# Optimization experiments

Hardware: AMD Instinct MI355X
Metric: run time of the kernel (lower is better)

The kernel has to match this reference:

```python
import jax, jax.numpy as jnp
import numpy as np
import math

D_MODEL = 1024
N_HEADS = 16
D_K = D_MODEL // N_HEADS
HIDDEN = 4096
R_SOFTPLUS_0 = 1.442695041
EPS = 1e-6


def setup_inputs() -> dict:
    key = jax.random.key(0)
    ks = jax.random.split(key, 16)
    B, S = 4, 2048
    s = 0.02
    inp = {
        "inputs": jax.random.normal(ks[0], (B, S, D_MODEL), jnp.float32),
        "mask": jnp.zeros((1, 1, S, S), jnp.float32),
        # RmsNorm (direct_scale=True -> init 1.0)
        "rms_scale": jnp.ones((D_MODEL,), jnp.float32),
        # attention projections (torch Linear: y = x @ W.T + b)
        "Wq": jax.random.normal(ks[1], (D_MODEL, D_MODEL), jnp.float32) * s,
        "bq": jnp.zeros((D_MODEL,), jnp.float32),
        "Wk": jax.random.normal(ks[2], (D_MODEL, D_MODEL), jnp.float32) * s,
        "bk": jnp.zeros((D_MODEL,), jnp.float32),
        "Wv": jax.random.normal(ks[3], (D_MODEL, D_MODEL), jnp.float32) * s,
        "bv": jnp.zeros((D_MODEL,), jnp.float32),
        "per_dim_scale": jnp.zeros((D_K,), jnp.float32),
        "Wpost": jax.random.normal(ks[4], (D_MODEL, D_MODEL), jnp.float32) * s,
        "bpost": jnp.zeros((D_MODEL,), jnp.float32),
        # FFN LayerNorm (direct_scale=False -> scale param init 0, effective 1+scale)
        "ln_scale": jnp.zeros((D_MODEL,), jnp.float32),
        "ln_bias": jnp.zeros((D_MODEL,), jnp.float32),
        "W1": jax.random.normal(ks[5], (HIDDEN, D_MODEL), jnp.float32) * s,
        "b1": jnp.zeros((HIDDEN,), jnp.float32),
        "W2": jax.random.normal(ks[6], (D_MODEL, HIDDEN), jnp.float32) * s,
        "b2": jnp.zeros((D_MODEL,), jnp.float32),
    }
    return inp


def _rms_norm(x, scale):
    ms = jnp.mean(x * x, axis=-1, keepdims=True)
    return x * jax.lax.rsqrt(ms + EPS) * scale


def _layer_norm(x, scale, bias):
    mean = jnp.mean(x, axis=-1, keepdims=True)
    var = jnp.mean((x - mean) ** 2, axis=-1, keepdims=True)
    return (x - mean) * jax.lax.rsqrt(var + EPS) * (1.0 + scale) + bias


def reference(inputs, mask, rms_scale, Wq, bq, Wk, bk, Wv, bv, per_dim_scale,
              Wpost, bpost, ln_scale, ln_bias, W1, b1, W2, b2):
    B, S, _ = inputs.shape
    x = _rms_norm(inputs, rms_scale)
    # projections -> [B, H, S, Dk]
    def split_heads(t):
        return t.reshape(B, S, N_HEADS, D_K).transpose(0, 2, 1, 3)
    q = split_heads(x @ Wq.T + bq)
    k = split_heads(x @ Wk.T + bk)
    v = split_heads(x @ Wv.T + bv)
    # PerDimScale: (r_softplus_0 / sqrt(d_k)) * softplus(param)
    scale = (R_SOFTPLUS_0 / math.sqrt(D_K)) * jax.nn.softplus(per_dim_scale)
    q = q * scale
    attn = jnp.einsum("bhqd,bhkd->bhqk", q, k) + mask
    attn = jax.nn.softmax(attn, axis=-1)
    out = jnp.einsum("bhqk,bhkd->bhqd", attn, v)
    out = out.transpose(0, 2, 1, 3).reshape(B, S, D_MODEL)
    attn_out = out @ Wpost.T + bpost
    h = attn_out + inputs  # residual (dropout=0)
    # FeedForward with pre-LayerNorm and residual
    y = _layer_norm(h, ln_scale, ln_bias)
    y = jax.nn.relu(y @ W1.T + b1)
    y = y @ W2.T + b2
    return y + h
```

## Files before the change

kernel.cpp:

```cpp
#include <hip/hip_runtime.h>
#include <hip/hip_bf16.h>

typedef unsigned short u16;
typedef __attribute__((ext_vector_type(8))) short short8;
typedef __attribute__((ext_vector_type(4))) float floatx4;

#define R_PDS 0.18033688f
#define LOG2E 1.4426950408889634f

__device__ __forceinline__ float bf2f(u16 u) {
    union { float f; unsigned int i; } c; c.i = ((unsigned int)u) << 16; return c.f;
}
__device__ __forceinline__ u16 f2b(float f) {
    union { float f; unsigned int i; } c; c.f = f;
    unsigned int r = c.i + 0x7fffu + ((c.i >> 16) & 1u);
    return (u16)(r >> 16);
}
__device__ __forceinline__ unsigned int pk2(float a, float b) {
    __hip_bfloat162 h = __float22bfloat162_rn(float2{a, b});
    unsigned int u; __builtin_memcpy(&u, &h, 4); return u;
}

__device__ __forceinline__ void async16(const u16* g, u16* l) {
    __builtin_amdgcn_global_load_lds(
        (const __attribute__((address_space(1))) unsigned int*)g,
        (__attribute__((address_space(3))) unsigned int*)l, 16, 0, 0);
}

__global__ __launch_bounds__(256) void f2b_all_k(const float* __restrict__ Wq, const float* __restrict__ Wk,
                                                 const float* __restrict__ Wv, const float* __restrict__ Wp,
                                                 const float* __restrict__ W1, const float* __restrict__ W2,
                                                 u16* __restrict__ Wqkvb, u16* __restrict__ Wpb,
                                                 u16* __restrict__ W1b,  u16* __restrict__ W2b,
                                                 int* flag) {
    int bid = blockIdx.x;
    if (bid == 0 && threadIdx.x == 0) *flag = 0;
    const float* src; u16* dst; int off;
    if      (bid < 1024) { src = Wq; dst = Wqkvb;                off = bid; }
    else if (bid < 2048) { src = Wk; dst = Wqkvb + 1024 * 1024;  off = bid - 1024; }
    else if (bid < 3072) { src = Wv; dst = Wqkvb + 2048 * 1024;  off = bid - 2048; }
    else if (bid < 4096) { src = Wp; dst = Wpb;                  off = bid - 3072; }
    else if (bid < 8192) { src = W1; dst = W1b;                  off = bid - 4096; }
    else                 { src = W2; dst = W2b;                  off = bid - 8192; }
    int i = off * 256 + threadIdx.x;
    float4 v = ((const float4*)src)[i];
    uint2 w; w.x = pk2(v.x, v.y); w.y = pk2(v.z, v.w);
    ((uint2*)dst)[i] = w;
}

__global__ __launch_bounds__(256) void mask_any_k(const float* __restrict__ mask, int* flag) {
    int i = blockIdx.x * 256 + threadIdx.x;
    uint4 u = ((const uint4*)mask)[i];
    unsigned int v = (u.x | u.y | u.z | u.w) & 0x7fffffffu;
    if (v) atomicOr(flag, 1);
}

__global__ __launch_bounds__(256) void rmsnorm_k(const float* __restrict__ in,
                                                 const float* __restrict__ gscale,
                                                 u16* __restrict__ out) {
    int row = blockIdx.x;
    int t = threadIdx.x, lane = t & 63, wave = t >> 6;
    const float* x = in + (size_t)row * 1024;
    float4 v = *(const float4*)(x + t * 4);
    float ss = v.x*v.x + v.y*v.y + v.z*v.z + v.w*v.w;
    for (int o = 1; o < 64; o <<= 1) ss += __shfl_xor(ss, o, 64);
    __shared__ float red[4];
    if (lane == 0) red[wave] = ss;
    __syncthreads();
    float tot = red[0] + red[1] + red[2] + red[3];
    float inv = rsqrtf(tot * (1.0f / 1024.0f) + 1e-6f);
    float4 s = *(const float4*)(gscale + t * 4);
    uint2 w;
    w.x = pk2(v.x * inv * s.x, v.y * inv * s.y);
    w.y = pk2(v.z * inv * s.z, v.w * inv * s.w);
    *(uint2*)(out + (size_t)row * 1024 + t * 4) = w;
}

__global__ __launch_bounds__(256) void layernorm_k(const u16* __restrict__ in,
                                                   const float* __restrict__ gs,
                                                   const float* __restrict__ gb,
                                                   u16* __restrict__ out) {
    int row = blockIdx.x;
    int t = threadIdx.x, lane = t & 63, wave = t >> 6;
    const u16* x = in + (size_t)row * 1024;
    uint2 u = *(const uint2*)(x + t * 4);
    float v0 = bf2f((u16)(u.x & 0xffff)), v1 = bf2f((u16)(u.x >> 16));
    float v2 = bf2f((u16)(u.y & 0xffff)), v3 = bf2f((u16)(u.y >> 16));
    float s1 = v0 + v1 + v2 + v3;
    float s2 = v0*v0 + v1*v1 + v2*v2 + v3*v3;
    for (int o = 1; o < 64; o <<= 1) { s1 += __shfl_xor(s1, o, 64); s2 += __shfl_xor(s2, o, 64); }
    __shared__ float r1[4], r2[4];
    if (lane == 0) { r1[wave] = s1; r2[wave] = s2; }
    __syncthreads();
    float mean = (r1[0] + r1[1] + r1[2] + r1[3]) * (1.0f / 1024.0f);
    float var  = (r2[0] + r2[1] + r2[2] + r2[3]) * (1.0f / 1024.0f) - mean * mean;
    var = fmaxf(var, 0.0f);
    float inv = rsqrtf(var + 1e-6f);
    float4 sc = *(const float4*)(gs + t * 4);
    float4 bb = *(const float4*)(gb + t * 4);
    uint2 w;
    w.x = pk2((v0 - mean) * inv * (1.0f + sc.x) + bb.x,
              (v1 - mean) * inv * (1.0f + sc.y) + bb.y);
    w.y = pk2((v2 - mean) * inv * (1.0f + sc.z) + bb.z,
              (v3 - mean) * inv * (1.0f + sc.w) + bb.w);
    *(uint2*)(out + (size_t)row * 1024 + t * 4) = w;
}

__device__ __forceinline__ void gemm8_core(const u16* __restrict__ A, const u16* __restrict__ B,
                                           int K, int NG, int m0, int n0,
                                           u16* lds, floatx4 (&acc)[8][4]) {
    const int t = threadIdx.x, wave = t >> 6, lane = t & 63;
    const int quad = lane >> 4, ln = lane & 15;
    const int wave_m = wave >> 2, wave_n = wave & 3;

    const int rowS = t >> 3;
    const int srcb = ((t & 7) * 16) ^ (((t >> 3) & 7) << 4);
    const u16* Ab = A + (size_t)(m0 + rowS) * K + (srcb >> 1);
    const u16* Bb = B + (size_t)(n0 + rowS) * K + (srcb >> 1);
    const size_t rstep = (size_t)64 * K;
    const size_t hstep = (size_t)128 * K;
    const int ldw = wave * 512;

    #define STAGE_A8(buf, h, kt) do { \
        u16* _l = lds + (buf) * 32768 + (h) * 8192 + ldw; \
        const u16* _g = Ab + (size_t)(h) * hstep + (kt); \
        async16(_g, _l); async16(_g + rstep, _l + 4096); } while (0)
    #define STAGE_B8(buf, h, kt) do { \
        u16* _l = lds + (buf) * 32768 + 16384 + (h) * 8192 + ldw; \
        const u16* _g = Bb + (size_t)(h) * hstep + (kt); \
        async16(_g, _l); async16(_g + rstep, _l + 4096); } while (0)

    #define RD8(base, lr, ks) \
        (*(const short8*)((base) + (lr) * 64 + ((((ks) * 64 + quad * 16) ^ (((lr) & 7) << 4)) >> 1)))

    STAGE_B8(0, 0, 0); STAGE_B8(0, 1, 0);
    STAGE_A8(0, 0, 0); STAGE_A8(0, 1, 0);
    if (NG > 1) {
        STAGE_B8(1, 0, 64); STAGE_B8(1, 1, 64);
        asm volatile("s_waitcnt vmcnt(4)" ::: "memory");
    } else {
        asm volatile("s_waitcnt vmcnt(0)" ::: "memory");
    }
    __builtin_amdgcn_s_barrier();

    for (int g = 0; g < NG; ++g) {
        const int cur = g & 1;
        const u16* aH = lds + cur * 32768 + wave_m * 8192;
        const u16* bH = lds + cur * 32768 + 16384 + (wave_n >> 1) * 8192;
        const int lrB = (wave_n & 1) * 64;
        short8 bf[4][2];
        #pragma unroll
        for (int q = 0; q < 4; ++q) {
            short8 af[2][2];
            #pragma unroll
            for (int mt = 0; mt < 2; ++mt)
                #pragma unroll
                for (int ks = 0; ks < 2; ++ks)
                    af[mt][ks] = RD8(aH, q * 32 + mt * 16 + ln, ks);
            if (q == 0) {
                #pragma unroll
                for (int nt = 0; nt < 4; ++nt)
                    #pragma unroll
                    for (int ks = 0; ks < 2; ++ks)
                        bf[nt][ks] = RD8(bH, lrB + nt * 16 + ln, ks);
            }
            if (q == 0 && g + 1 < NG) STAGE_A8(cur ^ 1, 0, (g + 1) * 64);
            if (q == 1 && g + 1 < NG) STAGE_A8(cur ^ 1, 1, (g + 1) * 64);
            if (q == 2 && g + 2 < NG) STAGE_B8(cur, 0, (g + 2) * 64);
            if (q == 3 && g + 2 < NG) STAGE_B8(cur, 1, (g + 2) * 64);
            __builtin_amdgcn_s_barrier();
            asm volatile("s_waitcnt lgkmcnt(0)" ::: "memory");
            __builtin_amdgcn_s_setprio(1);
            #pragma unroll
            for (int ks = 0; ks < 2; ++ks)
                #pragma unroll
                for (int mt = 0; mt < 2; ++mt)
                    #pragma unroll
                    for (int nt = 0; nt < 4; ++nt)
                        acc[q * 2 + mt][nt] = __builtin_amdgcn_mfma_f32_16x16x32_bf16(
                            af[mt][ks], bf[nt][ks], acc[q * 2 + mt][nt], 0, 0, 0);
            __builtin_amdgcn_s_setprio(0);
            __builtin_amdgcn_sched_barrier(0);
            if (q == 3 && g + 1 < NG) {
                if (g + 2 < NG) asm volatile("s_waitcnt vmcnt(4)" ::: "memory");
                else            asm volatile("s_waitcnt vmcnt(0)" ::: "memory");
            }
            __builtin_amdgcn_s_barrier();
        }
    }
    #undef STAGE_A8
    #undef STAGE_B8
    #undef RD8
}

__device__ __forceinline__ void xcd_swizzle(int& bx, int& by) {
    int gx = gridDim.x, nwg = gx * gridDim.y;
    int lin = blockIdx.y * gx + blockIdx.x;
    int swz = (lin & 7) * (nwg >> 3) + (lin >> 3);
    bx = swz % gx; by = swz / gx;
}

template <int EPI, bool OUTF32, bool RESF32>
__global__ __launch_bounds__(512, 2) void gemm8_bt_k(const u16* __restrict__ A,
                                                     const u16* __restrict__ B,
                                                     const float* __restrict__ bias,
                                                     const void* __restrict__ res,
                                                     void* __restrict__ Cv,
                                                     int M, int N, int K) {
    __shared__ __align__(16) u16 lds[65536];
    int bx, by; xcd_swizzle(bx, by);
    const int m0 = by * 256, n0 = bx * 256;
    const int t = threadIdx.x, wave = t >> 6, lane = t & 63;
    const int quad = lane >> 4, ln = lane & 15;
    const int wm = (wave >> 2) * 128, wn = (wave & 3) * 64;

    floatx4 acc[8][4];
    #pragma unroll
    for (int mf = 0; mf < 8; mf++)
        #pragma unroll
        for (int nf = 0; nf < 4; nf++) acc[mf][nf] = (floatx4)0.0f;

    gemm8_core(A, B, K, K >> 6, m0, n0, lds, acc);

    #pragma unroll
    for (int nf = 0; nf < 4; nf++) {
        int col = n0 + wn + nf * 16 + ln;
        float bv = bias[col];
        #pragma unroll
        for (int mf = 0; mf < 8; mf++) {
            int row = m0 + wm + mf * 16 + quad * 4;
            #pragma unroll
            for (int r = 0; r < 4; r++) {
                float v = acc[mf][nf][r] + bv;
                if (EPI == 1) v = fmaxf(v, 0.0f);
                if (EPI == 2) {
                    if (RESF32) v += ((const float*)res)[(size_t)(row + r) * N + col];
                    else        v += bf2f(((const u16*)res)[(size_t)(row + r) * N + col]);
                }
                if (OUTF32) ((float*)Cv)[(size_t)(row + r) * N + col] = v;
                else        ((u16*)Cv)[(size_t)(row + r) * N + col] = f2b(v);
            }
        }
    }
}

__global__ __launch_bounds__(512, 2) void gemm8_qkv_k(const u16* __restrict__ A,
                                                      const u16* __restrict__ B,
                                                      const float* __restrict__ bq,
                                                      const float* __restrict__ bk,
                                                      const float* __restrict__ bv,
                                                      const float* __restrict__ pds,
                                                      u16* __restrict__ C) {
    const int K = 1024, N = 3072;
    __shared__ __align__(16) u16 lds[65536];
    int bx, by; xcd_swizzle(bx, by);
    const int m0 = by * 256, n0 = bx * 256;
    const int t = threadIdx.x, wave = t >> 6, lane = t & 63;
    const int quad = lane >> 4, ln = lane & 15;
    const int wm = (wave >> 2) * 128, wn = (wave & 3) * 64;

    floatx4 acc[8][4];
    #pragma unroll
    for (int mf = 0; mf < 8; mf++)
        #pragma unroll
        for (int nf = 0; nf < 4; nf++) acc[mf][nf] = (floatx4)0.0f;

    gemm8_core(A, B, K, K >> 6, m0, n0, lds, acc);

    #pragma unroll
    for (int nf = 0; nf < 4; nf++) {
        int col = n0 + wn + nf * 16 + ln;
        float bv_, sc = 1.0f;
        if (col < 1024) {
            bv_ = bq[col];
            float xp = pds[col & 63];
            float sp = (xp > 20.0f) ? xp : log1pf(__expf(xp));
            sc = R_PDS * sp * LOG2E;
        } else if (col < 2048) bv_ = bk[col - 1024];
        else                   bv_ = bv[col - 2048];
        #pragma unroll
        for (int mf = 0; mf < 8; mf++) {
            int row = m0 + wm + mf * 16 + quad * 4;
            #pragma unroll
            for (int r = 0; r < 4; r++)
                C[(size_t)(row + r) * N + col] = f2b((acc[mf][nf][r] + bv_) * sc);
        }
    }
}

__global__ __launch_bounds__(256) void transpose_v_k(const u16* __restrict__ qkv, u16* __restrict__ vT) {
    __shared__ u16 tile[64][65];
    int st = blockIdx.x, bh = blockIdx.y;
    int b = bh >> 4, h = bh & 15;
    const u16* vb = qkv + (size_t)(b * 2048 + st * 64) * 3072 + 2048 + h * 64;
    int t = threadIdx.x;
    for (int i = t; i < 4096; i += 256) {
        int s = i >> 6, d = i & 63;
        tile[s][d] = vb[(size_t)s * 3072 + d];
    }
    __syncthreads();
    u16* ob = vT + (size_t)bh * 131072 + st * 64;
    for (int i = t; i < 4096; i += 256) {
        int d = i >> 6, s = i & 63;
        ob[(size_t)d * 2048 + s] = tile[s][d];
    }
}

__global__ __launch_bounds__(256) void attn_k(const u16* __restrict__ qkv,
                                              const u16* __restrict__ vT,
                                              const float* __restrict__ mask,
                                              const int* __restrict__ flag,
                                              u16* __restrict__ o) {
    __shared__ __align__(16) u16 QPs[128][72];
    __shared__ __align__(16) u16 Ks[64][72];
    __shared__ __align__(16) u16 Vs[64][72];

    const int t = threadIdx.x, wave = t >> 6, lane = t & 63;
    const int quad = lane >> 4, ln = lane & 15;
    const int qt = blockIdx.x, bh = blockIdx.y;
    const int b = bh >> 4, h = bh & 15;
    const int q0 = qt * 128;
    const int wm = wave * 32;

    const u16* qb = qkv + (size_t)(b * 2048 + q0) * 3072 + h * 64;
    for (int c = t; c < 1024; c += 256) {
        int row = c >> 3, seg = c & 7;
        *(uint4*)&QPs[row][seg * 8] = *(const uint4*)(qb + (size_t)row * 3072 + seg * 8);
    }
    __syncthreads();

    short8 qf[2][2];
    for (int mt = 0; mt < 2; mt++)
        for (int ks = 0; ks < 2; ks++)
            qf[mt][ks] = *(const short8*)&QPs[wm + mt * 16 + ln][ks * 32 + quad * 8];

    short8 ones_f;
    for (int i = 0; i < 8; i++) ones_f[i] = (short)0x3F80;

    floatx4 acc_o[2][4], acc_l[2];
    for (int mt = 0; mt < 2; mt++) {
        acc_l[mt] = (floatx4)0.0f;
        for (int dt = 0; dt < 4; dt++) acc_o[mt][dt] = (floatx4)0.0f;
    }

    const int mflag = *flag;
    const u16* kb = qkv + (size_t)(b * 2048) * 3072 + 1024 + h * 64;
    const u16* vg = vT + (size_t)bh * 131072;

    const int r0 = t >> 3, s0 = (t & 7) * 8;
    const u16* kp0 = kb + (size_t)r0 * 3072 + s0;
    const u16* kp1 = kb + (size_t)(r0 + 32) * 3072 + s0;
    const u16* vp0 = vg + (size_t)r0 * 2048 + s0;
    const u16* vp1 = vg + (size_t)(r0 + 32) * 2048 + s0;

    uint4 kr0 = *(const uint4*)(kp0);
    uint4 kr1 = *(const uint4*)(kp1);
    uint4 vr0 = *(const uint4*)(vp0);
    uint4 vr1 = *(const uint4*)(vp1);

    for (int kv0 = 0; kv0 < 2048; kv0 += 64) {
        __syncthreads();
        *(uint4*)&Ks[r0][s0]      = kr0;
        *(uint4*)&Ks[r0 + 32][s0] = kr1;
        *(uint4*)&Vs[r0][s0]      = vr0;
        *(uint4*)&Vs[r0 + 32][s0] = vr1;
        __syncthreads();
        if (kv0 + 64 < 2048) {
            size_t ko = (size_t)(kv0 + 64) * 3072;
            int    vo = kv0 + 64;
            kr0 = *(const uint4*)(kp0 + ko);
            kr1 = *(const uint4*)(kp1 + ko);
            vr0 = *(const uint4*)(vp0 + vo);
            vr1 = *(const uint4*)(vp1 + vo);
        }

        for (int nt = 0; nt < 4; nt++) {
            floatx4 sa0 = (floatx4)0.0f, sa1 = (floatx4)0.0f;
            for (int ks = 0; ks < 2; ks++) {
                short8 kf = *(const short8*)&Ks[nt * 16 + ln][ks * 32 + quad * 8];
                sa0 = __builtin_amdgcn_mfma_f32_16x16x32_bf16(kf, qf[0][ks], sa0, 0, 0, 0);
                sa1 = __builtin_amdgcn_mfma_f32_16x16x32_bf16(kf, qf[1][ks], sa1, 0, 0, 0);
            }
            if (mflag) {
                for (int r = 0; r < 4; r++) {
                    int kc = kv0 + nt * 16 + quad * 4 + r;
                    sa0[r] += mask[(size_t)(q0 + wm + ln) * 2048 + kc] * LOG2E;
                    sa1[r] += mask[(size_t)(q0 + wm + 16 + ln) * 2048 + kc] * LOG2E;
                }
            }
            {
                uint2 w;
                w.x = pk2(__builtin_amdgcn_exp2f(fminf(sa0[0], 80.0f)),
                          __builtin_amdgcn_exp2f(fminf(sa0[1], 80.0f)));
                w.y = pk2(__builtin_amdgcn_exp2f(fminf(sa0[2], 80.0f)),
                          __builtin_amdgcn_exp2f(fminf(sa0[3], 80.0f)));
                *(uint2*)&QPs[wm + ln][nt * 16 + quad * 4] = w;
            }
            {
                uint2 w;
                w.x = pk2(__builtin_amdgcn_exp2f(fminf(sa1[0], 80.0f)),
                          __builtin_amdgcn_exp2f(fminf(sa1[1], 80.0f)));
                w.y = pk2(__builtin_amdgcn_exp2f(fminf(sa1[2], 80.0f)),
                          __builtin_amdgcn_exp2f(fminf(sa1[3], 80.0f)));
                *(uint2*)&QPs[wm + 16 + ln][nt * 16 + quad * 4] = w;
            }
        }

        for (int ks = 0; ks < 2; ks++) {
            short8 a0 = *(const short8*)&QPs[wm + ln][ks * 32 + quad * 8];
            short8 a1 = *(const short8*)&QPs[wm + 16 + ln][ks * 32 + quad * 8];
            acc_l[0] = __builtin_amdgcn_mfma_f32_16x16x32_bf16(a0, ones_f, acc_l[0], 0, 0, 0);
            acc_l[1] = __builtin_amdgcn_mfma_f32_16x16x32_bf16(a1, ones_f, acc_l[1], 0, 0, 0);
            for (int dt = 0; dt < 4; dt++) {
                short8 bfr = *(const short8*)&Vs[dt * 16 + ln][ks * 32 + quad * 8];
                acc_o[0][dt] = __builtin_amdgcn_mfma_f32_16x16x32_bf16(a0, bfr, acc_o[0][dt], 0, 0, 0);
                acc_o[1][dt] = __builtin_amdgcn_mfma_f32_16x16x32_bf16(a1, bfr, acc_o[1][dt], 0, 0, 0);
            }
        }
    }

    u16* ob = o + (size_t)(b * 2048 + q0) * 1024 + h * 64;
    for (int mt = 0; mt < 2; mt++) {
        for (int r = 0; r < 4; r++) {
            float inv = 1.0f / acc_l[mt][r];
            int row = wm + mt * 16 + quad * 4 + r;
            for (int dt = 0; dt < 4; dt++)
                ob[(size_t)row * 1024 + dt * 16 + ln] = f2b(acc_o[mt][dt][r] * inv);
        }
    }
}

extern "C" void kernel_launch(void* const* d_in, const int* in_sizes, int n_in,
                              void* d_out, int out_size, void* d_ws, size_t ws_size,
                              hipStream_t stream) {
    const float* inp    = (const float*)d_in[0];
    const float* mask   = (const float*)d_in[1];
    const float* rms_s  = (const float*)d_in[2];
    const float* Wq     = (const float*)d_in[3];
    const float* bq     = (const float*)d_in[4];
    const float* Wk     = (const float*)d_in[5];
    const float* bk     = (const float*)d_in[6];
    const float* Wv     = (const float*)d_in[7];
    const float* bv     = (const float*)d_in[8];
    const float* pds    = (const float*)d_in[9];
    const float* Wpost  = (const float*)d_in[10];
    const float* bpost  = (const float*)d_in[11];
    const float* ln_s   = (const float*)d_in[12];
    const float* ln_b   = (const float*)d_in[13];
    const float* W1     = (const float*)d_in[14];
    const float* b1     = (const float*)d_in[15];
    const float* W2     = (const float*)d_in[16];
    const float* b2     = (const float*)d_in[17];
    float* out = (float*)d_out;

    char* w = (char*)d_ws;
    const size_t MB = 1u << 20;
    u16* W1b   = (u16*)(w + 0 * MB);
    u16* W2b   = (u16*)(w + 8 * MB);
    u16* qkv   = (u16*)(w + 16 * MB);
    u16* x     = (u16*)(w + 64 * MB);
    u16* o     = (u16*)(w + 64 * MB);
    u16* Wqkvb = (u16*)(w + 80 * MB);
    u16* Wpb   = (u16*)(w + 86 * MB);
    u16* yln   = (u16*)(w + 80 * MB);
    u16* vT    = (u16*)(w + 96 * MB);
    u16* hb    = (u16*)(w + 96 * MB);
    u16* f1    = (u16*)(w + 16 * MB);
    int* flag  = (int*)(w + 112 * MB);

    f2b_all_k<<<12288, 256, 0, stream>>>(Wq, Wk, Wv, Wpost, W1, W2, Wqkvb, Wpb, W1b, W2b, flag);
    mask_any_k<<<4096, 256, 0, stream>>>(mask, flag);

    rmsnorm_k<<<8192, 256, 0, stream>>>(inp, rms_s, x);

    gemm8_qkv_k<<<dim3(12, 32), 512, 0, stream>>>(x, Wqkvb, bq, bk, bv, pds, qkv);

    transpose_v_k<<<dim3(32, 64), 256, 0, stream>>>(qkv, vT);

    attn_k<<<dim3(16, 64), 256, 0, stream>>>(qkv, vT, mask, flag, o);

    gemm8_bt_k<2, false, true><<<dim3(4, 32), 512, 0, stream>>>(o, Wpb, bpost, inp, hb, 8192, 1024, 1024);

    layernorm_k<<<8192, 256, 0, stream>>>(hb, ln_s, ln_b, yln);

    gemm8_bt_k<1, false, true><<<dim3(16, 32), 512, 0, stream>>>(yln, W1b, b1, nullptr, f1, 8192, 4096, 1024);
    gemm8_bt_k<2, true, false><<<dim3(4, 32), 512, 0, stream>>>(f1, W2b, b2, hb, out, 8192, 1024, 4096);
}
```

Before: 600.6 us.

## Add 128x256 tile GEMM variant for QKV, output projection and FFN down GEMMs

Introduces a half-height (128-row) tile GEMM core with its own LDS layout and double-buffered async staging. The core is used for the QKV, post-attention and W2 projections, doubling the workgroup count so the N=1024 GEMMs fill more compute units. It trades lower per-tile data reuse and more global traffic for better occupancy across the device. It also adds a scheduling barrier after the LDS wait in the existing core.

```diff
diff --git a/kernel.cpp b/kernel.cpp
--- a/kernel.cpp
+++ b/kernel.cpp
@@ -106,6 +106,13 @@
     *(uint2*)(out + (size_t)row * 1024 + t * 4) = w;
 }
 
+__device__ __forceinline__ void xcd_swizzle(int& bx, int& by) {
+    int gx = gridDim.x, nwg = gx * gridDim.y;
+    int lin = blockIdx.y * gx + blockIdx.x;
+    int swz = (lin & 7) * (nwg >> 3) + (lin >> 3);
+    bx = swz % gx; by = swz / gx;
+}
+
 __device__ __forceinline__ void gemm8_core(const u16* __restrict__ A, const u16* __restrict__ B,
                                            int K, int NG, int m0, int n0,
                                            u16* lds, floatx4 (&acc)[8][4]) {
@@ -170,6 +177,7 @@
             if (q == 3 && g + 2 < NG) STAGE_B8(cur, 1, (g + 2) * 64);
             __builtin_amdgcn_s_barrier();
             asm volatile("s_waitcnt lgkmcnt(0)" ::: "memory");
+            __builtin_amdgcn_sched_barrier(0);
             __builtin_amdgcn_s_setprio(1);
             #pragma unroll
             for (int ks = 0; ks < 2; ++ks)
@@ -193,11 +201,88 @@
     #undef RD8
 }
 
-__device__ __forceinline__ void xcd_swizzle(int& bx, int& by) {
-    int gx = gridDim.x, nwg = gx * gridDim.y;
-    int lin = blockIdx.y * gx + blockIdx.x;
-    int swz = (lin & 7) * (nwg >> 3) + (lin >> 3);
-    bx = swz % gx; by = swz / gx;
+__device__ __forceinline__ void gemm8h_core(const u16* __restrict__ A, const u16* __restrict__ B,
+                                            int K, int NG, int m0, int n0,
+                                            u16* lds, floatx4 (&acc)[4][4]) {
+    const int t = threadIdx.x, wave = t >> 6, lane = t & 63;
+    const int quad = lane >> 4, ln = lane & 15;
+    const int wm = (wave >> 2) * 64, wn = (wave & 3) * 64;
+
+    const int rowS = t >> 3;
+    const int srcb = ((t & 7) * 16) ^ (((t >> 3) & 7) << 4);
+    const u16* Ab = A + (size_t)(m0 + rowS) * K + (srcb >> 1);
+    const u16* Bb = B + (size_t)(n0 + rowS) * K + (srcb >> 1);
+    const size_t hstep = (size_t)64 * K;
+    const int ldw = wave * 512;
+
+    #define STAGE_AH(buf, h, kt) \
+        async16(Ab + (size_t)(h) * hstep + (kt), lds + (buf) * 24576 + (h) * 4096 + ldw)
+    #define STAGE_BH(buf, h, kt) \
+        async16(Bb + (size_t)(h) * hstep + (kt), lds + (buf) * 24576 + 8192 + (h) * 4096 + ldw)
+    #define RD8H(base, lr, ks) \
+        (*(const short8*)((base) + (lr) * 64 + ((((ks) * 64 + quad * 16) ^ (((lr) & 7) << 4)) >> 1)))
+
+    STAGE_BH(0, 0, 0); STAGE_BH(0, 1, 0); STAGE_BH(0, 2, 0); STAGE_BH(0, 3, 0);
+    STAGE_AH(0, 0, 0); STAGE_AH(0, 1, 0);
+    if (NG > 1) {
+        STAGE_BH(1, 0, 64); STAGE_BH(1, 1, 64); STAGE_BH(1, 2, 64); STAGE_BH(1, 3, 64);
+        asm volatile("s_waitcnt vmcnt(4)" ::: "memory");
+    } else {
+        asm volatile("s_waitcnt vmcnt(0)" ::: "memory");
+    }
+    __builtin_amdgcn_s_barrier();
+
+    for (int g = 0; g < NG; ++g) {
+        const int cur = g & 1;
+        const u16* aB = lds + cur * 24576;
+        const u16* bB = lds + cur * 24576 + 8192;
+        short8 bf[4][2];
+        #pragma unroll
+        for (int q = 0; q < 2; ++q) {
+            short8 af[2][2];
+            #pragma unroll
+            for (int mt = 0; mt < 2; ++mt)
+                #pragma unroll
+                for (int ks = 0; ks < 2; ++ks)
+                    af[mt][ks] = RD8H(aB, wm + (q * 2 + mt) * 16 + ln, ks);
+            if (q == 0) {
+                #pragma unroll
+                for (int nt = 0; nt < 4; ++nt)
+                    #pragma unroll
+                    for (int ks = 0; ks < 2; ++ks)
+                        bf[nt][ks] = RD8H(bB, wn + nt * 16 + ln, ks);
+            }
+            if (q == 0 && g + 1 < NG) {
+                STAGE_AH(cur ^ 1, 0, (g + 1) * 64); STAGE_AH(cur ^ 1, 1, (g + 1) * 64);
+            }
+            if (q == 1 && g + 2 < NG) {
+                STAGE_BH(cur, 0, (g + 2) * 64); STAGE_BH(cur, 1, (g + 2) * 64);
+                STAGE_BH(cur, 2, (g + 2) * 64); STAGE_BH(cur, 3, (g + 2) * 64);
+            }
+            __builtin_amdgcn_s_barrier();
+            asm volatile("s_waitcnt lgkmcnt(0)" ::: "memory");
+            __builtin_amdgcn_sched_barrier(0);
+            __builtin_amdgcn_s_setprio(1);
+            #pragma unroll
+            for (int ks = 0; ks < 2; ++ks)
+                #pragma unroll
+                for (int mt = 0; mt < 2; ++mt)
+                    #pragma unroll
+                    for (int nt = 0; nt < 4; ++nt)
+                        acc[q * 2 + mt][nt] = __builtin_amdgcn_mfma_f32_16x16x32_bf16(
+                            af[mt][ks], bf[nt][ks], acc[q * 2 + mt][nt], 0, 0, 0);
+            __builtin_amdgcn_s_setprio(0);
+            __builtin_amdgcn_sched_barrier(0);
+            if (q == 1 && g + 1 < NG) {
+                if (g + 2 < NG) asm volatile("s_waitcnt vmcnt(4)" ::: "memory");
+                else            asm volatile("s_waitcnt vmcnt(0)" ::: "memory");
+            }
+            __builtin_amdgcn_s_barrier();
+        }
+    }
+    #undef STAGE_AH
+    #undef STAGE_BH
+    #undef RD8H
 }
 
 template <int EPI, bool OUTF32, bool RESF32>
@@ -244,28 +329,72 @@
     }
 }
 
-__global__ __launch_bounds__(512, 2) void gemm8_qkv_k(const u16* __restrict__ A,
+template <int EPI, bool OUTF32, bool RESF32>
+__global__ __launch_bounds__(512, 2) void gemm8h_bt_k(const u16* __restrict__ A,
                                                       const u16* __restrict__ B,
-                                                      const float* __restrict__ bq,
-                                                      const float* __restrict__ bk,
-                                                      const float* __restrict__ bv,
-                                                      const float* __restrict__ pds,
-                                                      u16* __restrict__ C) {
-    const int K = 1024, N = 3072;
-    __shared__ __align__(16) u16 lds[65536];
+                                                      const float* __restrict__ bias,
+                                                      const void* __restrict__ res,
+                                                      void* __restrict__ Cv,
+                                                      int M, int N, int K) {
+    __shared__ __align__(16) u16 lds[49152];
     int bx, by; xcd_swizzle(bx, by);
-    const int m0 = by * 256, n0 = bx * 256;
+    const int m0 = by * 128, n0 = bx * 256;
     const int t = threadIdx.x, wave = t >> 6, lane = t & 63;
     const int quad = lane >> 4, ln = lane & 15;
-    const int wm = (wave >> 2) * 128, wn = (wave & 3) * 64;
-
-    floatx4 acc[8][4];
+    const int wm = (wave >> 2) * 64, wn = (wave & 3) * 64;
+
+    floatx4 acc[4][4];
     #pragma unroll
-    for (int mf = 0; mf < 8; mf++)
+    for (int mf = 0; mf < 4; mf++)
         #pragma unroll
         for (int nf = 0; nf < 4; nf++) acc[mf][nf] = (floatx4)0.0f;
 
-    gemm8_core(A, B, K, K >> 6, m0, n0, lds, acc);
+    gemm8h_core(A, B, K, K >> 6, m0, n0, lds, acc);
+
+    #pragma unroll
+    for (int nf = 0; nf < 4; nf++) {
+        int col = n0 + wn + nf * 16 + ln;
+        float bv = bias[col];
+        #pragma unroll
+        for (int mf = 0; mf < 4; mf++) {
+            int row = m0 + wm + mf * 16 + quad * 4;
+            #pragma unroll
+            for (int r = 0; r < 4; r++) {
+                float v = acc[mf][nf][r] + bv;
+                if (EPI == 1) v = fmaxf(v, 0.0f);
+                if (EPI == 2) {
+                    if (RESF32) v += ((const float*)res)[(size_t)(row + r) * N + col];
+                    else        v += bf2f(((const u16*)res)[(size_t)(row + r) * N + col]);
+                }
+                if (OUTF32) ((float*)Cv)[(size_t)(row + r) * N + col] = v;
+                else        ((u16*)Cv)[(size_t)(row + r) * N + col] = f2b(v);
+            }
+        }
+    }
+}
+
+__global__ __launch_bounds__(512, 2) void gemm8h_qkv_k(const u16* __restrict__ A,
+                                                       const u16* __restrict__ B,
+                                                       const float* __restrict__ bq,
+                                                       const float* __restrict__ bk,
+                                                       const float* __restrict__ bv,
+                                                       const float* __restrict__ pds,
+                                                       u16* __restrict__ C) {
+    const int K = 1024, N = 3072;
+    __shared__ __align__(16) u16 lds[49152];
+    int bx, by; xcd_swizzle(bx, by);
+    const int m0 = by * 128, n0 = bx * 256;
+    const int t = threadIdx.x, wave = t >> 6, lane = t & 63;
+    const int quad = lane >> 4, ln = lane & 15;
+    const int wm = (wave >> 2) * 64, wn = (wave & 3) * 64;
+
+    floatx4 acc[4][4];
+    #pragma unroll
+    for (int mf = 0; mf < 4; mf++)
+        #pragma unroll
+        for (int nf = 0; nf < 4; nf++) acc[mf][nf] = (floatx4)0.0f;
+
+    gemm8h_core(A, B, K, K >> 6, m0, n0, lds, acc);
 
     #pragma unroll
     for (int nf = 0; nf < 4; nf++) {
@@ -279,7 +408,7 @@
         } else if (col < 2048) bv_ = bk[col - 1024];
         else                   bv_ = bv[col - 2048];
         #pragma unroll
-        for (int mf = 0; mf < 8; mf++) {
+        for (int mf = 0; mf < 4; mf++) {
             int row = m0 + wm + mf * 16 + quad * 4;
             #pragma unroll
             for (int r = 0; r < 4; r++)
@@ -473,16 +602,16 @@
 
     rmsnorm_k<<<8192, 256, 0, stream>>>(inp, rms_s, x);
 
-    gemm8_qkv_k<<<dim3(12, 32), 512, 0, stream>>>(x, Wqkvb, bq, bk, bv, pds, qkv);
+    gemm8h_qkv_k<<<dim3(12, 64), 512, 0, stream>>>(x, Wqkvb, bq, bk, bv, pds, qkv);
 
     transpose_v_k<<<dim3(32, 64), 256, 0, stream>>>(qkv, vT);
 
     attn_k<<<dim3(16, 64), 256, 0, stream>>>(qkv, vT, mask, flag, o);
 
-    gemm8_bt_k<2, false, true><<<dim3(4, 32), 512, 0, stream>>>(o, Wpb, bpost, inp, hb, 8192, 1024, 1024);
+    gemm8h_bt_k<2, false, true><<<dim3(4, 64), 512, 0, stream>>>(o, Wpb, bpost, inp, hb, 8192, 1024, 1024);
 
     layernorm_k<<<8192, 256, 0, stream>>>(hb, ln_s, ln_b, yln);
 
     gemm8_bt_k<1, false, true><<<dim3(16, 32), 512, 0, stream>>>(yln, W1b, b1, nullptr, f1, 8192, 4096, 1024);
-    gemm8_bt_k<2, true, false><<<dim3(4, 32), 512, 0, stream>>>(f1, W2b, b2, hb, out, 8192, 1024, 4096);
-}
+    gemm8h_bt_k<2, true, false><<<dim3(4, 64), 512, 0, stream>>>(f1, W2b, b2, hb, out, 8192, 1024, 4096);
+}
```

Measured after the change: 556.9 us. 1.08x faster.
